# Performance work log

Measured on AMD Instinct MI355X. Metric: run time of the kernel, lower is better.

The kernel has to match this reference:

```python
import jax, jax.numpy as jnp
import numpy as np

N, E, D = 100000, 600000, 128

def setup_inputs() -> dict:
    key = jax.random.key(0)
    ks = jax.random.split(key, 6)
    s = 1.0 / np.sqrt(D)
    return {
        "h": jax.random.normal(ks[0], (N, D), dtype=jnp.float32),
        "edge_index": jax.random.randint(ks[1], (2, E), 0, N, dtype=jnp.int64),
        "Wg": jax.random.normal(ks[2], (2 * D, D), dtype=jnp.float32) * s,
        "bg": jnp.zeros((D,), dtype=jnp.float32),
        "Ws": jax.random.normal(ks[3], (D, D), dtype=jnp.float32) * s,
        "bs": jnp.zeros((D,), dtype=jnp.float32),
        "Wr": jax.random.normal(ks[4], (D, D), dtype=jnp.float32) * s,
        "br": jnp.zeros((D,), dtype=jnp.float32),
    }

def reference(h, edge_index, Wg, bg, Ws, bs, Wr, br):
    send, rec = edge_index[0], edge_index[1]
    h_rec = h[rec]            # [E, D]
    h_send = h[send]          # [E, D]
    # gate: sigmoid(Linear(cat([h_rec, h_send])))  -- split W to avoid concat copy
    gate_in = h_rec @ Wg[:h.shape[1]] + h_send @ Wg[h.shape[1]:] + bg
    eta = jax.nn.sigmoid(gate_in)                      # [E, D]
    h_messages = eta * (h_send @ Ws + bs)              # [E, D]
    h_agg = jax.ops.segment_sum(h_messages, rec, num_segments=h.shape[0])
    return (h @ Wr + br) + h_agg
```

## Files before the change

### kernel.cpp

```cpp
#include <hip/hip_runtime.h>
#include <stdint.h>

#define FD 128

typedef __bf16 bf16x8 __attribute__((ext_vector_type(8)));
typedef unsigned short u16x8 __attribute__((ext_vector_type(8)));
typedef float  f32x16 __attribute__((ext_vector_type(16)));

__device__ __forceinline__ unsigned short f2bf(float f) {
    unsigned u = __float_as_uint(f);
    unsigned r = u + 0x7fffu + ((u >> 16) & 1u);
    return (unsigned short)(r >> 16);
}
__device__ __forceinline__ float bflo(unsigned u) { return __uint_as_float(u << 16); }
__device__ __forceinline__ float bfhi(unsigned u) { return __uint_as_float(u & 0xffff0000u); }

__global__ __launch_bounds__(256) void prep_kernel(
    const float* __restrict__ Wg,
    const float* __restrict__ Ws,
    const float* __restrict__ Wr,
    unsigned short* __restrict__ Wf)
{
    int wid = blockIdx.x * 256 + threadIdx.x;
    if (wid >= 512 * 128) return;
    int j  = wid & 7;
    int l  = (wid >> 3) & 63;
    int kt = (wid >> 9) & 7;
    int ct = wid >> 12;
    int k  = kt * 16 + (l >> 5) * 8 + j;
    int c  = ct * 32 + (l & 31);
    float v;
    if (c < 128)      v = Wg[k * FD + c];
    else if (c < 256) v = Wg[(128 + k) * FD + (c - 128)];
    else if (c < 384) v = Ws[k * FD + (c - 256)];
    else              v = Wr[k * FD + (c - 384)];
    Wf[wid] = f2bf(v);
}

__global__ __launch_bounds__(256, 2) void gemm_kernel(
    const float* __restrict__ h,
    const unsigned short* __restrict__ Wf,
    const float* __restrict__ bg,
    const float* __restrict__ bs,
    const float* __restrict__ br,
    unsigned short* __restrict__ A,
    unsigned short* __restrict__ B,
    unsigned short* __restrict__ S,
    float* __restrict__ out,
    int N)
{
    const int w    = threadIdx.x >> 6;
    const int lane = threadIdx.x & 63;

    bf16x8 barr[32];
    #pragma unroll
    for (int f = 0; f < 32; ++f)
        barr[f] = *(const bf16x8*)(Wf + (size_t)((w * 32 + f) * 64 + lane) * 8);

    const int col_l  = lane & 31;
    const int rhalf  = (lane >> 5) * 4;
    float bias[4];
    #pragma unroll
    for (int i = 0; i < 4; ++i) {
        int col = i * 32 + col_l;
        bias[i] = (w == 0) ? bg[col] : (w == 2) ? bs[col] : (w == 3) ? br[col] : 0.0f;
    }

    const int stride = gridDim.x * 32;
    for (int rb = blockIdx.x * 32; rb < N; rb += stride) {
        int arow = rb + (lane & 31);
        if (arow >= N) arow = N - 1;
        const float* aptr = h + (size_t)arow * FD + (lane >> 5) * 8;

        bf16x8 afrag[8];
        #pragma unroll
        for (int kt = 0; kt < 8; ++kt) {
            float4 f0 = *(const float4*)(aptr + kt * 16);
            float4 f1 = *(const float4*)(aptr + kt * 16 + 4);
            union { u16x8 u; bf16x8 b; } cv;
            cv.u[0] = f2bf(f0.x); cv.u[1] = f2bf(f0.y);
            cv.u[2] = f2bf(f0.z); cv.u[3] = f2bf(f0.w);
            cv.u[4] = f2bf(f1.x); cv.u[5] = f2bf(f1.y);
            cv.u[6] = f2bf(f1.z); cv.u[7] = f2bf(f1.w);
            afrag[kt] = cv.b;
        }

        f32x16 acc[4];
        #pragma unroll
        for (int i = 0; i < 4; ++i)
            #pragma unroll
            for (int r = 0; r < 16; ++r) acc[i][r] = 0.0f;

        #pragma unroll
        for (int kt = 0; kt < 8; ++kt) {
            #pragma unroll
            for (int i = 0; i < 4; ++i)
                acc[i] = __builtin_amdgcn_mfma_f32_32x32x16_bf16(
                             afrag[kt], barr[i * 8 + kt], acc[i], 0, 0, 0);
        }

        if (rb + 32 <= N) {
            #pragma unroll
            for (int i = 0; i < 4; ++i) {
                int col = i * 32 + col_l;
                #pragma unroll
                for (int r = 0; r < 16; ++r) {
                    int row = rb + (r & 3) + 8 * (r >> 2) + rhalf;
                    float v = acc[i][r] + bias[i];
                    size_t off = (size_t)row * FD + col;
                    if (w == 0)      A[off] = f2bf(v);
                    else if (w == 1) B[off] = f2bf(v);
                    else if (w == 2) S[off] = f2bf(v);
                    else             out[off] = v;
                }
            }
        } else {
            #pragma unroll
            for (int i = 0; i < 4; ++i) {
                int col = i * 32 + col_l;
                #pragma unroll
                for (int r = 0; r < 16; ++r) {
                    int row = rb + (r & 3) + 8 * (r >> 2) + rhalf;
                    if (row < N) {
                        float v = acc[i][r] + bias[i];
                        size_t off = (size_t)row * FD + col;
                        if (w == 0)      A[off] = f2bf(v);
                        else if (w == 1) B[off] = f2bf(v);
                        else if (w == 2) S[off] = f2bf(v);
                        else             out[off] = v;
                    }
                }
            }
        }
    }
}

__global__ __launch_bounds__(256) void hist_kernel(
    const int* __restrict__ idx, int* __restrict__ deg, int E)
{
    int e = blockIdx.x * 256 + threadIdx.x;
    if (e >= E) return;
    atomicAdd(&deg[idx[E + e]], 1);
}

__global__ __launch_bounds__(256) void scan1_kernel(
    const int* __restrict__ deg, int* __restrict__ partial, int N)
{
    __shared__ int sh[256];
    int base = blockIdx.x * 1024 + threadIdx.x * 4;
    int s = 0;
    #pragma unroll
    for (int j = 0; j < 4; ++j) s += (base + j < N) ? deg[base + j] : 0;
    sh[threadIdx.x] = s;
    __syncthreads();
    for (int ofs = 128; ofs > 0; ofs >>= 1) {
        if (threadIdx.x < ofs) sh[threadIdx.x] += sh[threadIdx.x + ofs];
        __syncthreads();
    }
    if (threadIdx.x == 0) partial[blockIdx.x] = sh[0];
}

__global__ __launch_bounds__(256) void scan2_kernel(int* __restrict__ partial, int nb)
{
    __shared__ int sh[256];
    int t = threadIdx.x;
    int p = (t < nb) ? partial[t] : 0;
    sh[t] = p;
    __syncthreads();
    for (int ofs = 1; ofs < 256; ofs <<= 1) {
        int x = (t >= ofs) ? sh[t - ofs] : 0;
        __syncthreads();
        sh[t] += x;
        __syncthreads();
    }
    if (t < nb) partial[t] = sh[t] - p;
}

__global__ __launch_bounds__(256) void scan3_kernel(
    int* __restrict__ deg, const int* __restrict__ partial, int N)
{
    __shared__ int sh[256];
    int base = blockIdx.x * 1024 + threadIdx.x * 4;
    int v[4];
    #pragma unroll
    for (int j = 0; j < 4; ++j) v[j] = (base + j < N) ? deg[base + j] : 0;
    int tsum = v[0] + v[1] + v[2] + v[3];
    sh[threadIdx.x] = tsum;
    __syncthreads();
    for (int ofs = 1; ofs < 256; ofs <<= 1) {
        int x = (threadIdx.x >= ofs) ? sh[threadIdx.x - ofs] : 0;
        __syncthreads();
        sh[threadIdx.x] += x;
        __syncthreads();
    }
    int run = partial[blockIdx.x] + sh[threadIdx.x] - tsum;
    #pragma unroll
    for (int j = 0; j < 4; ++j) {
        if (base + j < N) deg[base + j] = run;
        run += v[j];
    }
}

__global__ __launch_bounds__(256) void scatter_kernel(
    const int* __restrict__ idx, int* __restrict__ off,
    int* __restrict__ csr, int E)
{
    int e = blockIdx.x * 256 + threadIdx.x;
    if (e >= E) return;
    int s = idx[e];
    int r = idx[E + e];
    int pos = atomicAdd(&off[r], 1);
    csr[pos] = s;
}

__global__ __launch_bounds__(256) void aggregate_kernel(
    const int* __restrict__ off,
    const int* __restrict__ csr,
    const unsigned* __restrict__ A,
    const unsigned* __restrict__ B,
    const unsigned* __restrict__ S,
    float* __restrict__ out,
    int N)
{
    int r = blockIdx.x * 4 + (threadIdx.x >> 6);
    if (r >= N) return;
    int lane = threadIdx.x & 63;

    int start = (r == 0) ? 0 : off[r - 1];
    int end   = off[r];
    if (start >= end) return;

    unsigned ua = A[(size_t)r * 64 + lane];
    float a0 = bflo(ua), a1 = bfhi(ua);
    float acc0 = 0.0f, acc1 = 0.0f;

    int i = start;
    for (; i + 1 < end; i += 2) {
        int s0 = csr[i], s1 = csr[i + 1];
        unsigned ub0 = B[(size_t)s0 * 64 + lane];
        unsigned us0 = S[(size_t)s0 * 64 + lane];
        unsigned ub1 = B[(size_t)s1 * 64 + lane];
        unsigned us1 = S[(size_t)s1 * 64 + lane];
        float g00 = a0 + bflo(ub0), g01 = a1 + bfhi(ub0);
        float g10 = a0 + bflo(ub1), g11 = a1 + bfhi(ub1);
        acc0 += bflo(us0) * __builtin_amdgcn_rcpf(1.0f + __expf(-g00));
        acc1 += bfhi(us0) * __builtin_amdgcn_rcpf(1.0f + __expf(-g01));
        acc0 += bflo(us1) * __builtin_amdgcn_rcpf(1.0f + __expf(-g10));
        acc1 += bfhi(us1) * __builtin_amdgcn_rcpf(1.0f + __expf(-g11));
    }
    if (i < end) {
        int s0 = csr[i];
        unsigned ub0 = B[(size_t)s0 * 64 + lane];
        unsigned us0 = S[(size_t)s0 * 64 + lane];
        float g00 = a0 + bflo(ub0), g01 = a1 + bfhi(ub0);
        acc0 += bflo(us0) * __builtin_amdgcn_rcpf(1.0f + __expf(-g00));
        acc1 += bfhi(us0) * __builtin_amdgcn_rcpf(1.0f + __expf(-g01));
    }

    float2* o = (float2*)(out + (size_t)r * FD + 2 * lane);
    float2 cur = *o;
    cur.x += acc0;
    cur.y += acc1;
    *o = cur;
}

extern "C" void kernel_launch(void* const* d_in, const int* in_sizes, int n_in,
                              void* d_out, int out_size, void* d_ws, size_t ws_size,
                              hipStream_t stream)
{
    const float* h  = (const float*)d_in[0];
    const int*   ei = (const int*)d_in[1];
    const float* Wg = (const float*)d_in[2];
    const float* bg = (const float*)d_in[3];
    const float* Ws = (const float*)d_in[4];
    const float* bs = (const float*)d_in[5];
    const float* Wr = (const float*)d_in[6];
    const float* br = (const float*)d_in[7];
    float* out = (float*)d_out;

    const int N = in_sizes[0] / FD;
    const int E = in_sizes[1] / 2;

    unsigned short* Wf  = (unsigned short*)d_ws;
    unsigned short* Abf = Wf + 512 * FD;
    unsigned short* Bbf = Abf + (size_t)N * FD;
    unsigned short* Sbf = Bbf + (size_t)N * FD;
    int* deg     = (int*)(Sbf + (size_t)N * FD);
    int* partial = deg + N;
    int* csr     = partial + 256;

    size_t need = (size_t)(512 * FD + 3ull * N * FD) * 2 + ((size_t)N + 256 + E) * 4;
    if (ws_size < need) return;

    const int nb = (N + 1023) / 1024;
    if (nb > 256) return;

    hipMemsetAsync(deg, 0, (size_t)N * 4, stream);

    prep_kernel<<<(512 * FD + 255) / 256, 256, 0, stream>>>(Wg, Ws, Wr, Wf);
    gemm_kernel<<<512, 256, 0, stream>>>(h, Wf, bg, bs, br,
                                         Abf, Bbf, Sbf, out, N);
    hist_kernel<<<(E + 255) / 256, 256, 0, stream>>>(ei, deg, E);
    scan1_kernel<<<nb, 256, 0, stream>>>(deg, partial, N);
    scan2_kernel<<<1, 256, 0, stream>>>(partial, nb);
    scan3_kernel<<<nb, 256, 0, stream>>>(deg, partial, N);
    scatter_kernel<<<(E + 255) / 256, 256, 0, stream>>>(ei, deg, csr, E);
    aggregate_kernel<<<(N + 3) / 4, 256, 0, stream>>>(deg, csr,
                                                      (const unsigned*)Abf,
                                                      (const unsigned*)Bbf,
                                                      (const unsigned*)Sbf,
                                                      out, N);
}
```

Measured before the change: 332.2 us.

## Stage weight slices in LDS and split output column groups across grid y

Before, each wave held its 128-column weight slice in registers, and every block's four waves read the same 32-row tile of h, each producing a different output group. Now each block handles one output group (blockIdx.y) and loads that 32KB weight slice into LDS with global_load_lds. Its four waves process different 32-row tiles, and B fragments are read from LDS inside the MFMA loop. This frees many registers, allowing a higher occupancy bound. In exchange, h rows are now read four times across the grid instead of once per block, and each MFMA step adds LDS reads.

```diff
diff --git a/kernel.cpp b/kernel.cpp
--- a/kernel.cpp
+++ b/kernel.cpp
@@ -37,7 +37,7 @@
     Wf[wid] = f2bf(v);
 }
 
-__global__ __launch_bounds__(256, 2) void gemm_kernel(
+__global__ __launch_bounds__(256, 4) void gemm_kernel(
     const float* __restrict__ h,
     const unsigned short* __restrict__ Wf,
     const float* __restrict__ bg,
@@ -49,13 +49,23 @@
     float* __restrict__ out,
     int N)
 {
-    const int w    = threadIdx.x >> 6;
+    __shared__ unsigned short Bsh[16384];
+
+    const int w    = blockIdx.y;
     const int lane = threadIdx.x & 63;
-
-    bf16x8 barr[32];
-    #pragma unroll
-    for (int f = 0; f < 32; ++f)
-        barr[f] = *(const bf16x8*)(Wf + (size_t)((w * 32 + f) * 64 + lane) * 8);
+    const int wid  = threadIdx.x >> 6;
+
+    {
+        const unsigned short* src = Wf + (size_t)w * 16384 + (size_t)threadIdx.x * 8;
+        unsigned short* dst = Bsh + (size_t)threadIdx.x * 8;
+        #pragma unroll
+        for (int p = 0; p < 8; ++p) {
+            __builtin_amdgcn_global_load_lds(
+                (const __attribute__((address_space(1))) void*)(src + p * 2048),
+                (__attribute__((address_space(3))) void*)(dst + p * 2048),
+                16, 0, 0);
+        }
+    }
 
     const int col_l  = lane & 31;
     const int rhalf  = (lane >> 5) * 4;
@@ -66,8 +76,11 @@
         bias[i] = (w == 0) ? bg[col] : (w == 2) ? bs[col] : (w == 3) ? br[col] : 0.0f;
     }
 
-    const int stride = gridDim.x * 32;
-    for (int rb = blockIdx.x * 32; rb < N; rb += stride) {
+    __syncthreads();
+
+    const int stride = gridDim.x * 128;
+    for (int rb0 = blockIdx.x * 128; rb0 < N; rb0 += stride) {
+        const int rb = rb0 + wid * 32;
         int arow = rb + (lane & 31);
         if (arow >= N) arow = N - 1;
         const float* aptr = h + (size_t)arow * FD + (lane >> 5) * 8;
@@ -94,9 +107,11 @@
         #pragma unroll
         for (int kt = 0; kt < 8; ++kt) {
             #pragma unroll
-            for (int i = 0; i < 4; ++i)
+            for (int i = 0; i < 4; ++i) {
+                bf16x8 bfr = *(const bf16x8*)(Bsh + (size_t)((i * 8 + kt) * 64 + lane) * 8);
                 acc[i] = __builtin_amdgcn_mfma_f32_32x32x16_bf16(
-                             afrag[kt], barr[i * 8 + kt], acc[i], 0, 0, 0);
+                             afrag[kt], bfr, acc[i], 0, 0, 0);
+            }
         }
 
         if (rb + 32 <= N) {
@@ -298,8 +313,9 @@
     hipMemsetAsync(deg, 0, (size_t)N * 4, stream);
 
     prep_kernel<<<(512 * FD + 255) / 256, 256, 0, stream>>>(Wg, Ws, Wr, Wf);
-    gemm_kernel<<<512, 256, 0, stream>>>(h, Wf, bg, bs, br,
-                                         Abf, Bbf, Sbf, out, N);
+    dim3 ggrid(256, 4);
+    gemm_kernel<<<ggrid, 256, 0, stream>>>(h, Wf, bg, bs, br,
+                                           Abf, Bbf, Sbf, out, N);
     hist_kernel<<<(E + 255) / 256, 256, 0, stream>>>(ei, deg, E);
     scan1_kernel<<<nb, 256, 0, stream>>>(deg, partial, N);
     scan2_kernel<<<1, 256, 0, stream>>>(partial, nb);
```

New measurement: 307.8 us. 7.4% less time.
